# Optimization experiments

Hardware: AMD Instinct MI355X
Metric: run time of the kernel (lower is better)

## Reference

```python
import jax, jax.numpy as jnp
import numpy as np

N_FILTERS = 40
FILTER_SIZE = 401   # int(16000*25/1000), forced odd
POOL_STRIDE = 160   # int(16000*10/1000)
EPS = 1e-6
S_SMOOTH = 0.04     # fixed PCEN smoothing coefficient s
DELTA = 2.0         # fixed PCEN bias delta
R_MIN, R_MAX = 0.2, 1.0
HIDDEN = 32


def setup_inputs() -> dict:
    key = jax.random.key(0)
    ks = jax.random.split(key, 6)
    B, L = 8, 160000
    x = jax.random.normal(ks[0], (B, L), dtype=jnp.float32)
    # mel-initialized Gabor params (as in mel_filter_params)
    sr, fmin, fmax = 16000.0, 60.0, 7800.0
    min_mel = 1127.0 * np.log1p(fmin / 700.0)
    max_mel = 1127.0 * np.log1p(fmax / 700.0)
    peaks_mel = np.linspace(min_mel, max_mel, N_FILTERS + 2)
    peaks_hz = 700.0 * np.expm1(peaks_mel / 1127.0)
    center_freqs = jnp.asarray(peaks_hz[1:-1] * 2.0 * np.pi / sr, dtype=jnp.float32)
    z = np.sqrt(2.0 * np.log(2.0)) / np.pi
    bandwidths = jnp.asarray(z * sr / (peaks_hz[2:] - peaks_hz[:-2]), dtype=jnp.float32)
    pooling_widths = jnp.full((N_FILTERS,), 0.4, dtype=jnp.float32)
    # GRU (input_size=1, hidden=32) + head Linear(32,32)->ReLU->Linear(32,2)
    def gl(k, shape):
        return jax.random.normal(k, shape, dtype=jnp.float32) * 0.1
    w_ih = gl(ks[1], (3 * HIDDEN, 1))
    w_hh = gl(ks[2], (3 * HIDDEN, HIDDEN))
    b_ih = jnp.zeros((3 * HIDDEN,), jnp.float32)
    b_hh = jnp.zeros((3 * HIDDEN,), jnp.float32)
    hw1 = gl(ks[3], (32, HIDDEN)); hb1 = jnp.zeros((32,), jnp.float32)
    hw2 = gl(ks[4], (2, 32)); hb2 = jnp.zeros((2,), jnp.float32)
    return dict(x=x, center_freqs=center_freqs, bandwidths=bandwidths,
                pooling_widths=pooling_widths, w_ih=w_ih, w_hh=w_hh,
                b_ih=b_ih, b_hh=b_hh, hw1=hw1, hb1=hb1, hw2=hw2, hb2=hb2)


def _gabor_filterbank(x, center_freqs, bandwidths, pooling_widths):
    z = np.sqrt(2.0 * np.log(2.0)) / np.pi
    cf = jnp.clip(center_freqs, 0.0, np.pi)
    bw = jnp.clip(bandwidths, 4.0 * z, FILTER_SIZE * z)
    t = jnp.arange(-(FILTER_SIZE // 2), (FILTER_SIZE + 1) // 2, dtype=jnp.float32)
    denom = 1.0 / (jnp.sqrt(2.0 * np.pi) * bw)                        # [F]
    gauss = jnp.exp(-(t[None, :] ** 2) / (2.0 * bw[:, None] ** 2))    # [F,K]
    phase = cf[:, None] * t[None, :]                                  # [F,K]
    fr = denom[:, None] * gauss * jnp.cos(phase)
    fi = denom[:, None] * gauss * jnp.sin(phase)
    filt = jnp.concatenate([fr, fi], axis=0)[:, None, :]              # [2F,1,K]
    pad = FILTER_SIZE // 2
    y = jax.lax.conv_general_dilated(x[:, None, :], filt, (1,), [(pad, pad)])
    y = y ** 2
    y = y[:, :N_FILTERS] + y[:, N_FILTERS:]                           # squared modulus [B,F,L]
    pw = jnp.clip(pooling_widths, 2.0 / FILTER_SIZE, 0.5)
    tt = jnp.arange(FILTER_SIZE, dtype=jnp.float32) / (FILTER_SIZE - 1) - 0.5
    win = jnp.exp(-0.5 * (tt[None, :] / pw[:, None]) ** 2)[:, None, :]  # [F,1,K]
    y = jax.lax.conv_general_dilated(y, win, (POOL_STRIDE,), [(pad, pad)],
                                     feature_group_count=N_FILTERS)
    return y  # [B,F,T]


def _gru_cell(h, xin, w_ih, w_hh, b_ih, b_hh):
    gi = xin @ w_ih.T + b_ih   # [N,3H]
    gh = h @ w_hh.T + b_hh
    i_r, i_z, i_n = jnp.split(gi, 3, axis=-1)
    h_r, h_z, h_n = jnp.split(gh, 3, axis=-1)
    r = jax.nn.sigmoid(i_r + h_r)
    zz = jax.nn.sigmoid(i_z + h_z)
    n = jnp.tanh(i_n + r * h_n)
    return (1.0 - zz) * n + zz * h


def _adaptive_pcen(frames, w_ih, w_hh, b_ih, b_hh, hw1, hb1, hw2, hb2):
    B, F, T = frames.shape
    Xt = jnp.transpose(frames, (2, 0, 1))  # [T,B,F]

    def controller(x_prev, x_t):  # each [B,F] -> per-bin (alpha, r)
        xp = x_prev.reshape(-1, 1)
        xc = x_t.reshape(-1, 1)
        h = jnp.zeros((B * F, HIDDEN), frames.dtype)
        h = _gru_cell(h, xp, w_ih, w_hh, b_ih, b_hh)
        h = _gru_cell(h, xc, w_ih, w_hh, b_ih, b_hh)
        hid = jax.nn.relu(h @ hw1.T + hb1)
        logits = hid @ hw2.T + hb2  # [B*F,2]
        alpha = jax.nn.sigmoid(logits[:, 0]).reshape(B, F)
        r = (R_MIN + (R_MAX - R_MIN) * jax.nn.sigmoid(logits[:, 1])).reshape(B, F)
        return alpha, r

    def step(carry, X_t):
        M_prev, X_prev = carry
        alpha, r = controller(X_prev, X_t)
        M_t = (1.0 - S_SMOOTH) * M_prev + S_SMOOTH * X_t
        out = (X_t / (M_t + EPS) ** alpha + DELTA) ** r - DELTA ** r
        return (M_t, X_t), out

    init = (jnp.zeros((B, F), frames.dtype), Xt[0])
    _, outs = jax.lax.scan(step, init, Xt)
    return jnp.transpose(outs, (1, 2, 0))  # [B,F,T]


def reference(x, center_freqs, bandwidths, pooling_widths,
              w_ih, w_hh, b_ih, b_hh, hw1, hb1, hw2, hb2):
    frames = _gabor_filterbank(x, center_freqs, bandwidths, pooling_widths)
    return _adaptive_pcen(frames, w_ih, w_hh, b_ih, b_hh, hw1, hb1, hw2, hb2)
```

## Files before the change

### kernel.cpp

```cpp
#include <hip/hip_runtime.h>
#include <math.h>

#define NF 40
#define FS 401
#define AST 424
#define PSTRIDE 160
#define BB 8
#define LL 160000
#define PADL 256
#define LST 161024
#define TOUT 1000
#define NTILE 512
#define NCHUNKC 313
#define ROWCH 121
#define ROWST (ROWCH*8)
#define EROW 520
#define WL2 432
#define NCONVB 5032

typedef __attribute__((ext_vector_type(8))) _Float16 half8v;
typedef __attribute__((ext_vector_type(4))) _Float16 half4v;
typedef __attribute__((ext_vector_type(2))) _Float16 half2v;
typedef __attribute__((ext_vector_type(4))) float float4v;
typedef _Float16 f16;

__device__ __forceinline__ float sigm(float x) { return 1.0f / (1.0f + __expf(-x)); }
__device__ __forceinline__ float tanh_fast(float x) { return 1.0f - 2.0f / (__expf(2.0f * x) + 1.0f); }

__global__ __launch_bounds__(256) void prep_all(
    const float* __restrict__ x, const float* __restrict__ cf_,
    const float* __restrict__ bw_, const float* __restrict__ pw_,
    f16* __restrict__ xb, f16* __restrict__ Ag, float* __restrict__ Wg4f)
{
    int blk = blockIdx.x;
    if (blk < NCONVB) {
        int i = blk * 256 + threadIdx.x;
        int b = i / LST, o = i % LST;
        float v = 0.0f;
        if (o >= PADL && o < PADL + LL) v = x[b * LL + (o - PADL)];
        xb[i] = (f16)v;
        return;
    }
    if (blk < NCONVB + 80) {
        const float PI_F = 3.14159265358979323846f;
        int row = blk - NCONVB;
        int f = row >> 1, comp = row & 1;
        float Z = sqrtf(2.0f * logf(2.0f)) / PI_F;
        float cf = fminf(fmaxf(cf_[f], 0.0f), PI_F);
        float bw = fminf(fmaxf(bw_[f], 4.0f * Z), 401.0f * Z);
        float denom = 1.0f / (sqrtf(2.0f * PI_F) * bw);
        float inv2 = 1.0f / (2.0f * bw * bw);
        for (int k = threadIdx.x; k < AST; k += 256) {
            float v = 0.0f;
            if (k < FS) {
                float t = (float)(k - 200);
                float g = denom * expf(-(t * t) * inv2);
                float sv, cv;
                sincosf(cf * t, &sv, &cv);
                v = comp ? g * sv : g * cv;
            }
            Ag[row * AST + k] = (f16)v;
        }
        return;
    }
    int f = blk - (NCONVB + 80);
    float pw = fminf(fmaxf(pw_[f], 2.0f / 401.0f), 0.5f);
    float invpw = 1.0f / pw;
    for (int idx = threadIdx.x; idx < 4 * WL2; idx += 256) {
        int r = idx / WL2, p = idx - r * WL2;
        int k = p - 2 * r;
        float w = 0.0f;
        if (k >= 0 && k < FS) {
            float ttv = (float)k * (1.0f / 400.0f) - 0.5f;
            float u = ttv * invpw;
            w = expf(-0.5f * u * u);
        }
        Wg4f[(f * 4 + r) * WL2 + p] = w;
    }
}

__global__ __launch_bounds__(256, 2) void conv_pool(
    const f16* __restrict__ xb,
    const f16* __restrict__ Ag,
    const float* __restrict__ Wg4f,
    float* __restrict__ Pp)
{
    __shared__ __align__(16) unsigned char smem[40 * EROW * 2];
    f16* slab = (f16*)smem;
    f16* eL   = (f16*)smem;

    int chunk = blockIdx.x;
    int bi = blockIdx.y;
    int p0 = chunk * NTILE;
    int pbase = PADL + p0 - 200;
    const f16* xs = xb + (size_t)bi * LST;
    int tid = threadIdx.x;

    for (int sc = tid; sc < 8 * 120; sc += 256) {
        int r = sc / 120, m = sc - r * 120;
        int s0 = pbase + 8 * m + (r & ~1);
        const uint* gp = (const uint*)(xs + s0);
        uint v0 = gp[0], v1 = gp[1], v2 = gp[2], v3 = gp[3], v4 = gp[4];
        if (r & 1) {
            v0 = __builtin_amdgcn_alignbyte(v1, v0, 2);
            v1 = __builtin_amdgcn_alignbyte(v2, v1, 2);
            v2 = __builtin_amdgcn_alignbyte(v3, v2, 2);
            v3 = __builtin_amdgcn_alignbyte(v4, v3, 2);
        }
        *(uint4*)(&slab[r * ROWST + 8 * m]) = make_uint4(v0, v1, v2, v3);
    }
    __syncthreads();

    int wv = tid >> 6, lane = tid & 63, q = lane >> 4, l15 = lane & 15;

    float4v acc[5][8];
#pragma unroll
    for (int t = 0; t < 5; ++t)
#pragma unroll
        for (int s = 0; s < 8; ++s)
            acc[t][s] = (float4v){0.f, 0.f, 0.f, 0.f};

    const f16* aP[5];
    const f16* bPtr[10];
#pragma unroll
    for (int t = 0; t < 5; ++t) aP[t] = Ag + (16 * t + l15) * AST + 8 * q;
#pragma unroll
    for (int s = 0; s < 10; ++s) {
        int pos = 128 * wv + 16 * s + l15;
        bPtr[s] = slab + (pos & 7) * ROWST + 8 * ((pos >> 3) + q);
    }

    half8v bf[8];
#pragma unroll
    for (int s = 0; s < 8; ++s) bf[s] = *(const half8v*)(bPtr[s]);

#pragma unroll
    for (int kk = 0; kk < 13; ++kk) {
        int k = 32 * kk;
        half8v af[5];
#pragma unroll
        for (int t = 0; t < 5; ++t) af[t] = *(const half8v*)(aP[t] + k);
        half8v nb0, nb1;
        if (kk < 12) {
            nb0 = *(const half8v*)(bPtr[8] + k);
            nb1 = *(const half8v*)(bPtr[9] + k);
        }
#pragma unroll
        for (int t = 0; t < 5; ++t)
#pragma unroll
            for (int s = 0; s < 8; ++s)
                acc[t][s] = __builtin_amdgcn_mfma_f32_16x16x32_f16(af[t], bf[s], acc[t][s], 0, 0, 0);
        if (kk < 12) {
#pragma unroll
            for (int s = 0; s < 6; ++s) bf[s] = bf[s + 2];
            bf[6] = nb0; bf[7] = nb1;
        }
    }

    __syncthreads();

#pragma unroll
    for (int t = 0; t < 5; ++t) {
        int f0 = 8 * t + 2 * q;
#pragma unroll
        for (int s = 0; s < 8; ++s) {
            float4v a = acc[t][s];
            int pl = 128 * wv + 16 * s + l15;
            bool ok = (p0 + pl) < LL;
            eL[f0 * EROW + pl] = ok ? (f16)(a.x * a.x + a.y * a.y) : (f16)0.f;
            eL[(f0 + 1) * EROW + pl] = ok ? (f16)(a.z * a.z + a.w * a.w) : (f16)0.f;
        }
    }
    for (int i = tid; i < 40 * 8; i += 256) {
        int r = i >> 3, cc = 512 + (i & 7);
        eL[r * EROW + cc] = (f16)0.f;
    }
    __syncthreads();

    int tau_lo = (p0 - 41) / 160;
    if (tau_lo < 0) tau_lo = 0;
    int tau_hi = (p0 + 711) / 160;
    if (tau_hi > TOUT - 1) tau_hi = TOUT - 1;
    int npr = (tau_hi - tau_lo + 1) * 40;
    int slot = chunk & 1;
    int gid = tid >> 4;
    int lg = tid & 15;

    for (int pr = gid; pr < npr; pr += 16) {
        int ta = pr / 40;
        int f = pr - ta * 40;
        int tau = tau_lo + ta;
        int b = tau * 160 - 200 - p0;
        int bc = b > 0 ? b : 0;
        int j0 = bc >> 3;
        int r = (b & 7) >> 1;
        int pw0 = 8 * j0 - b + 2 * r;
        int jlast = (b + 400) >> 3;
        if (jlast > 64) jlast = 64;
        const f16* ebase = eL + f * EROW;
        const float* wbase = Wg4f + ((f * 4 + r) * WL2) + pw0;
        float4v pac0 = {0.f, 0.f, 0.f, 0.f};
        float4v pac1 = {0.f, 0.f, 0.f, 0.f};
#pragma unroll
        for (int i = 0; i < 4; ++i) {
            int j = j0 + 16 * i + lg;
            bool act = (j <= jlast);
            int jc = act ? j : j0;
            half8v e8 = *(const half8v*)(ebase + 8 * jc);
            const float* wp = wbase + 8 * (jc - j0);
            float4v w0 = *(const float4v*)(wp);
            float4v w1 = *(const float4v*)(wp + 4);
            if (act) {
                pac0.x = fmaf((float)e8[0], w0.x, pac0.x);
                pac0.y = fmaf((float)e8[1], w0.y, pac0.y);
                pac0.z = fmaf((float)e8[2], w0.z, pac0.z);
                pac0.w = fmaf((float)e8[3], w0.w, pac0.w);
                pac1.x = fmaf((float)e8[4], w1.x, pac1.x);
                pac1.y = fmaf((float)e8[5], w1.y, pac1.y);
                pac1.z = fmaf((float)e8[6], w1.z, pac1.z);
                pac1.w = fmaf((float)e8[7], w1.w, pac1.w);
            }
        }
        float pa = ((pac0.x + pac0.y) + (pac0.z + pac0.w))
                 + ((pac1.x + pac1.y) + (pac1.z + pac1.w));
        pa += __shfl_xor(pa, 1, 16);
        pa += __shfl_xor(pa, 2, 16);
        pa += __shfl_xor(pa, 4, 16);
        pa += __shfl_xor(pa, 8, 16);
        if (lg == 0)
            Pp[(((size_t)bi * TOUT + tau) * NF + f) * 2 + slot] = pa;
    }
}

__global__ __launch_bounds__(256) void pcen_scan_kernel(
    const float* __restrict__ Pp, float* __restrict__ X, float* __restrict__ M)
{
    int wid = (blockIdx.x * 256 + threadIdx.x) >> 6;
    int lane = threadIdx.x & 63;
    if (wid >= BB * NF) return;
    const float a1 = 0.96f;
    const float a2 = a1 * a1;
    const float a4 = a2 * a2;
    const float a8 = a4 * a4;
    const float a16 = a8 * a8;
    const float a32 = a16 * a16;
    const float ss = 0.04f;
    float al1 = powf(a1, (float)(lane + 1));
    float carry = 0.0f;
    int bi = wid / NF, f = wid - bi * NF;
    const float* pbase = Pp + (size_t)bi * TOUT * NF * 2 + f * 2;
    float* xrow = X + (size_t)wid * TOUT;
    float* mrow = M + (size_t)wid * TOUT;

    for (int c = 0; c < TOUT; c += 64) {
        int t = c + lane;
        float v = 0.0f;
        if (t < TOUT) {
            int s = t * 160 - 200;
            int cl = (s > 0) ? (s >> 9) : 0;
            int ch = (s + 400) >> 9;
            if (ch > NCHUNKC - 1) ch = NCHUNKC - 1;
            v = pbase[(size_t)t * NF * 2 + (cl & 1)];
            if (ch > cl) v += pbase[(size_t)t * NF * 2 + ((cl & 1) ^ 1)];
            xrow[t] = v;
        }
        float y = ss * v;
        float u;
        u = __shfl_up(y, 1, 64);  if (lane >= 1)  y = fmaf(a1, u, y);
        u = __shfl_up(y, 2, 64);  if (lane >= 2)  y = fmaf(a2, u, y);
        u = __shfl_up(y, 4, 64);  if (lane >= 4)  y = fmaf(a4, u, y);
        u = __shfl_up(y, 8, 64);  if (lane >= 8)  y = fmaf(a8, u, y);
        u = __shfl_up(y, 16, 64); if (lane >= 16) y = fmaf(a16, u, y);
        u = __shfl_up(y, 32, 64); if (lane >= 32) y = fmaf(a32, u, y);
        y = fmaf(al1, carry, y);
        carry = __shfl(y, 63, 64);
        if (t < TOUT) mrow[t] = y;
    }
}

__global__ __launch_bounds__(256) void pcen_ctrl_mfma(
    const float* __restrict__ X, const float* __restrict__ M,
    const float* __restrict__ w_ih, const float* __restrict__ w_hh,
    const float* __restrict__ b_ih, const float* __restrict__ b_hh,
    const float* __restrict__ hw1, const float* __restrict__ hb1,
    const float* __restrict__ hw2, const float* __restrict__ hb2,
    float* __restrict__ out)
{
    __shared__ f16 s_whhA[96 * 40];
    __shared__ f16 s_w1A[32 * 40];
    __shared__ __align__(16) float4 s_A1[32];
    __shared__ __align__(16) float4 s_A2[32];
    __shared__ float s_hb1[32];
    __shared__ float s_hw2[64];
    __shared__ float s_hb2[2];
    __shared__ f16 sh1[4][16 * 40];
    __shared__ f16 sh2[4][16 * 40];
    __shared__ float sxc[4][16], sxp[4][16], smv[4][16];

    int tid = threadIdx.x;
    for (int i = tid; i < 96 * 32; i += 256) {
        int m = i >> 5, k = i & 31;
        s_whhA[m * 40 + k] = (f16)w_hh[i];
    }
    for (int i = tid; i < 32 * 32; i += 256) {
        int m = i >> 5, k = i & 31;
        s_w1A[m * 40 + k] = (f16)hw1[i];
    }
    if (tid < 32) {
        int j = tid;
        s_A1[j] = make_float4(w_ih[j], b_ih[j] + b_hh[j],
                              w_ih[32 + j], b_ih[32 + j] + b_hh[32 + j]);
        s_A2[j] = make_float4(w_ih[64 + j], b_ih[64 + j], b_hh[64 + j], 0.0f);
        s_hb1[j] = hb1[j];
    }
    if (tid < 64) s_hw2[tid] = hw2[tid];
    if (tid < 2)  s_hb2[tid] = hb2[tid];
    __syncthreads();

    int wv = tid >> 6, lane = tid & 63;
    int c = lane & 15, q = lane >> 4;

    for (int rep = 0; rep < 8; ++rep) {
        int instBase = blockIdx.x * 512 + rep * 64 + wv * 16;

        if (lane < 16) {
            int idx = instBase + lane;
            int t = idx % TOUT;
            float xcv = X[idx];
            float xpv = (t == 0) ? xcv : X[idx - 1];
            sxc[wv][lane] = xcv;
            sxp[wv][lane] = xpv;
            smv[wv][lane] = M[idx];
        }
        float xp = sxp[wv][c];
        float xc = sxc[wv][c];
        float mv = smv[wv][c];

        float h1v[8];
#pragma unroll
        for (int jj = 0; jj < 8; ++jj) {
            int j = (jj < 4) ? (4 * q + jj) : (16 + 4 * q + (jj - 4));
            float4 a1 = s_A1[j];
            float4 a2 = s_A2[j];
            float r = sigm(fmaf(xp, a1.x, a1.y));
            float z = sigm(fmaf(xp, a1.z, a1.w));
            float n = tanh_fast(fmaf(xp, a2.x, a2.y) + r * a2.z);
            h1v[jj] = (1.0f - z) * n;
        }

        {
            half4v lo = {(f16)h1v[0], (f16)h1v[1], (f16)h1v[2], (f16)h1v[3]};
            half4v hi = {(f16)h1v[4], (f16)h1v[5], (f16)h1v[6], (f16)h1v[7]};
            *(half4v*)(&sh1[wv][c * 40 + 4 * q]) = lo;
            *(half4v*)(&sh1[wv][c * 40 + 16 + 4 * q]) = hi;
        }

        float4v acc[6];
        {
            half8v bf = *(const half8v*)(&sh1[wv][c * 40 + 8 * q]);
#pragma unroll
            for (int t = 0; t < 6; ++t) {
                half8v af = *(const half8v*)(&s_whhA[(16 * t + c) * 40 + 8 * q]);
                acc[t] = __builtin_amdgcn_mfma_f32_16x16x32_f16(af, bf, (float4v){0.f,0.f,0.f,0.f}, 0, 0, 0);
            }
        }

        float h2v[8];
#pragma unroll
        for (int jj = 0; jj < 8; ++jj) {
            int j = (jj < 4) ? (4 * q + jj) : (16 + 4 * q + (jj - 4));
            int reg = jj & 3;
            float accR = (jj < 4) ? acc[0][reg] : acc[1][reg];
            float accZ = (jj < 4) ? acc[2][reg] : acc[3][reg];
            float accN = (jj < 4) ? acc[4][reg] : acc[5][reg];
            float4 a1 = s_A1[j];
            float4 a2 = s_A2[j];
            float r = sigm(fmaf(xc, a1.x, a1.y) + accR);
            float z = sigm(fmaf(xc, a1.z, a1.w) + accZ);
            float gn = accN + a2.z;
            float n = tanh_fast(fmaf(xc, a2.x, a2.y) + r * gn);
            h2v[jj] = fmaf(z, h1v[jj] - n, n);
        }

        {
            half4v lo = {(f16)h2v[0], (f16)h2v[1], (f16)h2v[2], (f16)h2v[3]};
            half4v hi = {(f16)h2v[4], (f16)h2v[5], (f16)h2v[6], (f16)h2v[7]};
            *(half4v*)(&sh2[wv][c * 40 + 4 * q]) = lo;
            *(half4v*)(&sh2[wv][c * 40 + 16 + 4 * q]) = hi;
        }

        float4v hacc[2];
        {
            half8v bf = *(const half8v*)(&sh2[wv][c * 40 + 8 * q]);
#pragma unroll
            for (int t = 0; t < 2; ++t) {
                half8v af = *(const half8v*)(&s_w1A[(16 * t + c) * 40 + 8 * q]);
                hacc[t] = __builtin_amdgcn_mfma_f32_16x16x32_f16(af, bf, (float4v){0.f,0.f,0.f,0.f}, 0, 0, 0);
            }
        }

        float p0 = 0.f, p1 = 0.f;
#pragma unroll
        for (int jj = 0; jj < 8; ++jj) {
            int i = (jj < 4) ? (4 * q + jj) : (16 + 4 * q + (jj - 4));
            int reg = jj & 3;
            float hv = (jj < 4) ? hacc[0][reg] : hacc[1][reg];
            hv = fmaxf(hv + s_hb1[i], 0.0f);
            p0 = fmaf(hv, s_hw2[i], p0);
            p1 = fmaf(hv, s_hw2[32 + i], p1);
        }
        p0 += __shfl_xor(p0, 16);
        p0 += __shfl_xor(p0, 32);
        p1 += __shfl_xor(p1, 16);
        p1 += __shfl_xor(p1, 32);

        float alpha = sigm(p0 + s_hb2[0]);
        float rr = fmaf(0.8f, sigm(p1 + s_hb2[1]), 0.2f);
        float md = __expf(alpha * __logf(mv + 1e-6f));
        float bse = xc / md + 2.0f;
        float val = __expf(rr * __logf(bse)) - __expf(rr * 0.69314718056f);
        if (lane < 16)
            out[instBase + lane] = val;
    }
}

extern "C" void kernel_launch(void* const* d_in, const int* in_sizes, int n_in,
                              void* d_out, int out_size, void* d_ws, size_t ws_size,
                              hipStream_t stream) {
    const float* x    = (const float*)d_in[0];
    const float* cf   = (const float*)d_in[1];
    const float* bw   = (const float*)d_in[2];
    const float* pw   = (const float*)d_in[3];
    const float* w_ih = (const float*)d_in[4];
    const float* w_hh = (const float*)d_in[5];
    const float* b_ih = (const float*)d_in[6];
    const float* b_hh = (const float*)d_in[7];
    const float* hw1  = (const float*)d_in[8];
    const float* hb1  = (const float*)d_in[9];
    const float* hw2  = (const float*)d_in[10];
    const float* hb2  = (const float*)d_in[11];
    float* out = (float*)d_out;

    f16* xb     = (f16*)d_ws;
    f16* Ag     = xb + (size_t)BB * LST;
    float* Wg4f = (float*)(Ag + (size_t)80 * AST);
    float* Pp   = Wg4f + (size_t)NF * 4 * WL2;
    float* Xf   = Pp + (size_t)BB * TOUT * NF * 2;
    float* Mf   = Xf + (size_t)BB * NF * TOUT;

    prep_all<<<dim3(NCONVB + 80 + 40), dim3(256), 0, stream>>>(
        x, cf, bw, pw, xb, Ag, Wg4f);

    conv_pool<<<dim3(NCHUNKC, BB), dim3(256), 0, stream>>>(xb, Ag, Wg4f, Pp);

    pcen_scan_kernel<<<dim3((BB * NF * 64) / 256), dim3(256), 0, stream>>>(Pp, Xf, Mf);
    pcen_ctrl_mfma<<<dim3((BB * NF * TOUT) / 512), dim3(256), 0, stream>>>(
        Xf, Mf, w_ih, w_hh, b_ih, b_hh, hw1, hb1, hw2, hb2, out);
}
```

Before: 285.3 us.

## Stage fp16 pooling window in LDS per filter half instead of global fp32 shifted copies

The pooling weights change from four shift-replicated fp32 rows per filter in global memory to a single fp16 row per filter. conv_pool copies these rows into shared memory in two halves of 20 filters and reads them from LDS. The aim is to cut global/L2 traffic for the pooling stage, at the cost of extra shared memory, which may lower occupancy. It also adds barriers, reads the weights as unaligned half2 values from LDS, and stores the window in fp16, which loses precision.

```diff
diff --git a/kernel.cpp b/kernel.cpp
--- a/kernel.cpp
+++ b/kernel.cpp
@@ -15,7 +15,7 @@
 #define ROWCH 121
 #define ROWST (ROWCH*8)
 #define EROW 520
-#define WL2 432
+#define WROW 424
 #define NCONVB 5032
 
 typedef __attribute__((ext_vector_type(8))) _Float16 half8v;
@@ -30,7 +30,7 @@
 __global__ __launch_bounds__(256) void prep_all(
     const float* __restrict__ x, const float* __restrict__ cf_,
     const float* __restrict__ bw_, const float* __restrict__ pw_,
-    f16* __restrict__ xb, f16* __restrict__ Ag, float* __restrict__ Wg4f)
+    f16* __restrict__ xb, f16* __restrict__ Ag, f16* __restrict__ Wf16)
 {
     int blk = blockIdx.x;
     if (blk < NCONVB) {
@@ -66,26 +66,26 @@
     int f = blk - (NCONVB + 80);
     float pw = fminf(fmaxf(pw_[f], 2.0f / 401.0f), 0.5f);
     float invpw = 1.0f / pw;
-    for (int idx = threadIdx.x; idx < 4 * WL2; idx += 256) {
-        int r = idx / WL2, p = idx - r * WL2;
-        int k = p - 2 * r;
+    for (int p = threadIdx.x; p < WROW; p += 256) {
+        int k = p - 8;
         float w = 0.0f;
         if (k >= 0 && k < FS) {
             float ttv = (float)k * (1.0f / 400.0f) - 0.5f;
             float u = ttv * invpw;
             w = expf(-0.5f * u * u);
         }
-        Wg4f[(f * 4 + r) * WL2 + p] = w;
+        Wf16[f * WROW + p] = (f16)w;
     }
 }
 
 __global__ __launch_bounds__(256, 2) void conv_pool(
     const f16* __restrict__ xb,
     const f16* __restrict__ Ag,
-    const float* __restrict__ Wg4f,
+    const f16* __restrict__ Wf16,
     float* __restrict__ Pp)
 {
     __shared__ __align__(16) unsigned char smem[40 * EROW * 2];
+    __shared__ __align__(16) f16 wt[20 * WROW];
     f16* slab = (f16*)smem;
     f16* eL   = (f16*)smem;
 
@@ -175,60 +175,74 @@
         int r = i >> 3, cc = 512 + (i & 7);
         eL[r * EROW + cc] = (f16)0.f;
     }
-    __syncthreads();
 
     int tau_lo = (p0 - 41) / 160;
     if (tau_lo < 0) tau_lo = 0;
     int tau_hi = (p0 + 711) / 160;
     if (tau_hi > TOUT - 1) tau_hi = TOUT - 1;
-    int npr = (tau_hi - tau_lo + 1) * 40;
+    int ntau = tau_hi - tau_lo + 1;
+    int b0 = tau_lo * 160 - 200 - p0;
     int slot = chunk & 1;
     int gid = tid >> 4;
     int lg = tid & 15;
 
-    for (int pr = gid; pr < npr; pr += 16) {
-        int ta = pr / 40;
-        int f = pr - ta * 40;
-        int tau = tau_lo + ta;
-        int b = tau * 160 - 200 - p0;
-        int bc = b > 0 ? b : 0;
-        int j0 = bc >> 3;
-        int r = (b & 7) >> 1;
-        int pw0 = 8 * j0 - b + 2 * r;
-        int jlast = (b + 400) >> 3;
-        if (jlast > 64) jlast = 64;
-        const f16* ebase = eL + f * EROW;
-        const float* wbase = Wg4f + ((f * 4 + r) * WL2) + pw0;
-        float4v pac0 = {0.f, 0.f, 0.f, 0.f};
-        float4v pac1 = {0.f, 0.f, 0.f, 0.f};
-#pragma unroll
-        for (int i = 0; i < 4; ++i) {
-            int j = j0 + 16 * i + lg;
-            bool act = (j <= jlast);
-            int jc = act ? j : j0;
-            half8v e8 = *(const half8v*)(ebase + 8 * jc);
-            const float* wp = wbase + 8 * (jc - j0);
-            float4v w0 = *(const float4v*)(wp);
-            float4v w1 = *(const float4v*)(wp + 4);
-            if (act) {
-                pac0.x = fmaf((float)e8[0], w0.x, pac0.x);
-                pac0.y = fmaf((float)e8[1], w0.y, pac0.y);
-                pac0.z = fmaf((float)e8[2], w0.z, pac0.z);
-                pac0.w = fmaf((float)e8[3], w0.w, pac0.w);
-                pac1.x = fmaf((float)e8[4], w1.x, pac1.x);
-                pac1.y = fmaf((float)e8[5], w1.y, pac1.y);
-                pac1.z = fmaf((float)e8[6], w1.z, pac1.z);
-                pac1.w = fmaf((float)e8[7], w1.w, pac1.w);
+    for (int half = 0; half < 2; ++half) {
+        {
+            const half8v* src = (const half8v*)(Wf16 + 20 * WROW * half);
+            half8v* dst = (half8v*)wt;
+            for (int i = tid; i < 20 * WROW / 8; i += 256)
+                dst[i] = src[i];
+        }
+        __syncthreads();
+
+        int nprh = ntau * 20;
+        int fi = gid;
+        int ta = 0;
+        for (int pr = gid; pr < nprh; pr += 16) {
+            int f = 20 * half + fi;
+            int tau = tau_lo + ta;
+            int b = b0 + 160 * ta;
+            int bc = b > 0 ? b : 0;
+            int j0 = bc >> 3;
+            int jlast = (b + 400) >> 3;
+            if (jlast > 64) jlast = 64;
+            const f16* ebase = eL + f * EROW;
+            int wbaseIdx = fi * WROW + 8 - b;
+            float4v pac0 = {0.f, 0.f, 0.f, 0.f};
+            float4v pac1 = {0.f, 0.f, 0.f, 0.f};
+#pragma unroll
+            for (int i = 0; i < 4; ++i) {
+                int j = j0 + 16 * i + lg;
+                bool act = (j <= jlast);
+                int jc = act ? j : j0;
+                half8v e8 = *(const half8v*)(ebase + 8 * jc);
+                const f16* wp = wt + wbaseIdx + 8 * jc;
+                half2v w0 = *(const half2v*)(wp);
+                half2v w1 = *(const half2v*)(wp + 2);
+                half2v w2 = *(const half2v*)(wp + 4);
+                half2v w3 = *(const half2v*)(wp + 6);
+                if (act) {
+                    pac0.x = fmaf((float)e8[0], (float)w0[0], pac0.x);
+                    pac0.y = fmaf((float)e8[1], (float)w0[1], pac0.y);
+                    pac0.z = fmaf((float)e8[2], (float)w1[0], pac0.z);
+                    pac0.w = fmaf((float)e8[3], (float)w1[1], pac0.w);
+                    pac1.x = fmaf((float)e8[4], (float)w2[0], pac1.x);
+                    pac1.y = fmaf((float)e8[5], (float)w2[1], pac1.y);
+                    pac1.z = fmaf((float)e8[6], (float)w3[0], pac1.z);
+                    pac1.w = fmaf((float)e8[7], (float)w3[1], pac1.w);
+                }
             }
-        }
-        float pa = ((pac0.x + pac0.y) + (pac0.z + pac0.w))
-                 + ((pac1.x + pac1.y) + (pac1.z + pac1.w));
-        pa += __shfl_xor(pa, 1, 16);
-        pa += __shfl_xor(pa, 2, 16);
-        pa += __shfl_xor(pa, 4, 16);
-        pa += __shfl_xor(pa, 8, 16);
-        if (lg == 0)
-            Pp[(((size_t)bi * TOUT + tau) * NF + f) * 2 + slot] = pa;
+            float pa = ((pac0.x + pac0.y) + (pac0.z + pac0.w))
+                     + ((pac1.x + pac1.y) + (pac1.z + pac1.w));
+            pa += __shfl_xor(pa, 1, 16);
+            pa += __shfl_xor(pa, 2, 16);
+            pa += __shfl_xor(pa, 4, 16);
+            pa += __shfl_xor(pa, 8, 16);
+            if (lg == 0)
+                Pp[(((size_t)bi * TOUT + tau) * NF + f) * 2 + slot] = pa;
+            fi += 16; if (fi >= 20) { fi -= 20; ++ta; }
+        }
+        __syncthreads();
     }
 }
 
@@ -441,17 +455,17 @@
     const float* hb2  = (const float*)d_in[11];
     float* out = (float*)d_out;
 
-    f16* xb     = (f16*)d_ws;
-    f16* Ag     = xb + (size_t)BB * LST;
-    float* Wg4f = (float*)(Ag + (size_t)80 * AST);
-    float* Pp   = Wg4f + (size_t)NF * 4 * WL2;
-    float* Xf   = Pp + (size_t)BB * TOUT * NF * 2;
-    float* Mf   = Xf + (size_t)BB * NF * TOUT;
+    f16* xb    = (f16*)d_ws;
+    f16* Ag    = xb + (size_t)BB * LST;
+    f16* Wf16  = Ag + (size_t)80 * AST;
+    float* Pp  = (float*)(Wf16 + (size_t)NF * WROW);
+    float* Xf  = Pp + (size_t)BB * TOUT * NF * 2;
+    float* Mf  = Xf + (size_t)BB * NF * TOUT;
 
     prep_all<<<dim3(NCONVB + 80 + 40), dim3(256), 0, stream>>>(
-        x, cf, bw, pw, xb, Ag, Wg4f);
-
-    conv_pool<<<dim3(NCHUNKC, BB), dim3(256), 0, stream>>>(xb, Ag, Wg4f, Pp);
+        x, cf, bw, pw, xb, Ag, Wf16);
+
+    conv_pool<<<dim3(NCHUNKC, BB), dim3(256), 0, stream>>>(xb, Ag, Wf16, Pp);
 
     pcen_scan_kernel<<<dim3((BB * NF * 64) / 256), dim3(256), 0, stream>>>(Pp, Xf, Mf);
     pcen_ctrl_mfma<<<dim3((BB * NF * TOUT) / 512), dim3(256), 0, stream>>>(
```

Result: faster. 267.2 us (-6.4%).
